# Optimization experiments

Hardware: AMD Instinct MI355X
Metric: run time of the kernel (lower is better)

Reference implementation:

```python
import jax, jax.numpy as jnp
import numpy as np

NEG_BIG = -9e15  # matches torch's -9000000000000000.0 mask value


def setup_inputs() -> dict:
    key = jax.random.key(0)
    k1, k2, k3, k4 = jax.random.split(key, 4)
    B, N, Din, Dout = 4, 4096, 256, 128
    x = jax.random.normal(k1, (B, N, Din), dtype=jnp.float32)
    adj = jax.random.randint(k2, (B, N, N), 0, 2, dtype=jnp.int32)
    weight = jax.random.normal(k3, (Din, Dout), dtype=jnp.float32) * (1.414 * (6.0 / (Din + Dout)) ** 0.5)
    a = jax.random.normal(k4, (2 * Dout, 1), dtype=jnp.float32) * 0.1
    bias = jnp.zeros((Dout,), dtype=jnp.float32)
    return {"x": x, "adj": adj, "weight": weight, "a": a, "bias": bias}


def reference(x, adj, weight, a, bias):
    Dout = weight.shape[1]
    h = jnp.matmul(x, weight)                       # [B, N, Dout]
    Wh1 = jnp.matmul(h, a[:Dout, :])                # [B, N, 1]
    Wh2 = jnp.matmul(h, a[Dout:, :])                # [B, N, 1]
    e = jax.nn.gelu(Wh1 + jnp.swapaxes(Wh2, 1, 2), approximate=False)  # [B, N, N]
    attention = jnp.where(adj > 0, e, NEG_BIG)
    attention = jax.nn.softmax(attention, axis=1)   # softmax over dim=1, as in torch code
    out = jnp.matmul(attention, h)                  # [B, N, Dout]
    out = jax.nn.gelu(out, approximate=False)
    # F.normalize(p=2, dim=1): L2-normalize over the node dimension
    norm = jnp.sqrt(jnp.sum(out * out, axis=1, keepdims=True))
    out = out / jnp.maximum(norm, 1e-12)
    return out + bias
```

## Files before the change

kernel.cpp:

```cpp
#include <hip/hip_runtime.h>
#include <hip/hip_bf16.h>
#include <stdint.h>


#define NN   4096
#define BB   4
#define DIN  256
#define DOUT 128

typedef unsigned short u16;
typedef _Float16 f16x8 __attribute__((ext_vector_type(8)));
typedef __attribute__((ext_vector_type(4))) float f32x4;

__device__ __forceinline__ u16 f2h_bits(float f) {
  _Float16 h = (_Float16)f;
  union { _Float16 h; u16 u; } v; v.h = h;
  return v.u;
}

__device__ __forceinline__ float erf_f(float x) {
  float ax = __builtin_fabsf(x);
  float t  = __builtin_amdgcn_rcpf(__builtin_fmaf(0.3275911f, ax, 1.0f));
  float p  = __builtin_fmaf(1.061405429f, t, -1.453152027f);
  p = __builtin_fmaf(p, t, 1.421413741f);
  p = __builtin_fmaf(p, t, -0.284496736f);
  p = __builtin_fmaf(p, t, 0.254829592f);
  p = p * t;
  float e  = __expf(-ax * ax);
  float er = __builtin_fmaf(-p, e, 1.0f);
  return copysignf(er, x);
}

__device__ __forceinline__ float gelu_f(float z) {
  float hz = 0.5f * z;
  return __builtin_fmaf(hz, erf_f(z * 0.70710678118654752f), hz);
}

__device__ __forceinline__ float exp_gelu(float z) { return __expf(gelu_f(z)); }

__global__ __launch_bounds__(256, 2) void k1_proj(
    const float* __restrict__ x, const float* __restrict__ weight,
    const float* __restrict__ a, u16* __restrict__ hT,
    float* __restrict__ Wh1, float* __restrict__ Wh2)
{
  __shared__ float xs[32 * 256];
  __shared__ float T[128 * 33];
  __shared__ float P2a[8 * 32], P2b[8 * 32];

  const int b = blockIdx.y, n0 = blockIdx.x * 32;
  const int tid = threadIdx.x;

  const float4* xsrc = (const float4*)(x + ((size_t)b * NN + n0) * DIN);
  float4* xd = (float4*)xs;
#pragma unroll
  for (int v = 0; v < 8; ++v) xd[tid + v * 256] = xsrc[tid + v * 256];
  __syncthreads();

  const int dg = tid & 31, rg = tid >> 5;
  float acc[4][4] = {};
  const float4* W4 = (const float4*)weight;
#pragma unroll 4
  for (int k = 0; k < 256; ++k) {
    float4 wr = W4[k * 32 + dg];
#pragma unroll
    for (int rr = 0; rr < 4; ++rr) {
      float xv = xs[(rg * 4 + rr) * 256 + k];
      acc[rr][0] = fmaf(xv, wr.x, acc[rr][0]);
      acc[rr][1] = fmaf(xv, wr.y, acc[rr][1]);
      acc[rr][2] = fmaf(xv, wr.z, acc[rr][2]);
      acc[rr][3] = fmaf(xv, wr.w, acc[rr][3]);
    }
  }
#pragma unroll
  for (int rr = 0; rr < 4; ++rr)
#pragma unroll
    for (int dd = 0; dd < 4; ++dd)
      T[(dg * 4 + dd) * 33 + rg * 4 + rr] = acc[rr][dd];
  __syncthreads();

  {
    const int d = tid & 127, half = tid >> 7;
    unsigned int uu[8];
#pragma unroll
    for (int p = 0; p < 8; ++p) {
      float f0 = T[d * 33 + half * 16 + p * 2];
      float f1 = T[d * 33 + half * 16 + p * 2 + 1];
      uu[p] = (unsigned int)f2h_bits(f0) | ((unsigned int)f2h_bits(f1) << 16);
    }
    u16* dst = hT + ((size_t)b * DOUT + d) * NN + n0 + half * 16;
    ((uint4*)dst)[0] = make_uint4(uu[0], uu[1], uu[2], uu[3]);
    ((uint4*)dst)[1] = make_uint4(uu[4], uu[5], uu[6], uu[7]);
  }
  {
    const int r = tid & 31, g8 = tid >> 5;
    float p1 = 0.f, p2 = 0.f;
#pragma unroll
    for (int q = 0; q < 16; ++q) {
      int d = g8 * 16 + q;
      float hv = T[d * 33 + r];
      p1 = fmaf(hv, a[d], p1);
      p2 = fmaf(hv, a[DOUT + d], p2);
    }
    P2a[g8 * 32 + r] = p1;
    P2b[g8 * 32 + r] = p2;
  }
  __syncthreads();
  if (tid < 32) {
    float s1 = 0.f, s2 = 0.f;
#pragma unroll
    for (int g8 = 0; g8 < 8; ++g8) { s1 += P2a[g8 * 32 + tid]; s2 += P2b[g8 * 32 + tid]; }
    Wh1[b * NN + n0 + tid] = s1;
    Wh2[b * NN + n0 + tid] = s2;
  }
}

__global__ __launch_bounds__(256) void k2a_mask(
    const int* __restrict__ adj, unsigned int* __restrict__ mask32)
{
  const int tid = threadIdx.x;
  const int row = blockIdx.x * 2 + (tid >> 7);
  const int w   = tid & 127;
  const int4* src = (const int4*)(adj + (size_t)row * NN) + w * 8;

  int4 v[8];
#pragma unroll
  for (int k = 0; k < 8; ++k) v[k] = src[k];

  unsigned int m = 0;
#pragma unroll
  for (int k = 0; k < 8; ++k) {
    m |= (v[k].x > 0 ? 1u : 0u) << (4 * k);
    m |= (v[k].y > 0 ? 1u : 0u) << (4 * k + 1);
    m |= (v[k].z > 0 ? 1u : 0u) << (4 * k + 2);
    m |= (v[k].w > 0 ? 1u : 0u) << (4 * k + 3);
  }
  mask32[(size_t)row * 128 + w] = m;
}

__global__ __launch_bounds__(256, 2) void k2b_colsum(
    const unsigned int* __restrict__ mask32, const float* __restrict__ Wh1,
    const float* __restrict__ Wh2, float* __restrict__ S)
{
  const int b = blockIdx.z, jt = blockIdx.x, ic = blockIdx.y;
  const int tid = threadIdx.x;
  const int j = jt * 256 + tid;
  const int i0 = ic * 256;
  const int jbit = tid & 31;

  const float wh2 = Wh2[b * NN + j];
  const unsigned int* mp = mask32 + ((size_t)b * NN + i0) * 128 + jt * 8 + (tid >> 5);
  const float* w1p = Wh1 + b * NN + i0;

  float s = 0.f;
  for (int g = 0; g < 32; ++g) {
    unsigned int mw[8];
    float w1v[8];
#pragma unroll
    for (int k = 0; k < 8; ++k) {
      mw[k]  = mp[(size_t)(g * 8 + k) * 128];
      w1v[k] = w1p[g * 8 + k];
    }
#pragma unroll
    for (int k = 0; k < 8; ++k) {
      float E = exp_gelu(w1v[k] + wh2);
      s += ((mw[k] >> jbit) & 1u) ? E : 0.f;
    }
  }
  atomicAdd(&S[b * NN + j], s);
}

__global__ __launch_bounds__(256) void k25_rcp(const float* __restrict__ S,
                                               float* __restrict__ Sinv)
{
  int id = blockIdx.x * 256 + threadIdx.x;
  Sinv[id] = 1.0f / S[id];
}

__global__ __launch_bounds__(256, 4) void k3_attn(
    const unsigned int* __restrict__ mask32, const float* __restrict__ Wh1,
    const float* __restrict__ Wh2, const float* __restrict__ Sinv,
    const u16* __restrict__ hT, float* __restrict__ out_pre)
{
  __shared__ __align__(16) u16 buf[4][128 * 32];

  const int b = blockIdx.y;
  const int i0 = blockIdx.x * 16;
  const int tid = threadIdx.x;
  const int w = tid >> 6, lane = tid & 63;
  const int m = lane & 15, quad = lane >> 4;
  const int i = i0 + m;

  const float w1 = Wh1[b * NN + i];
  const unsigned int* mrow = mask32 + ((size_t)b * NN + i) * 128;
  const u16* hTb = hT + (size_t)b * DOUT * NN;

  const u16* srcbase = hTb + (size_t)(lane >> 2) * NN + (lane & 3) * 8;

  f32x4 acc[8];
#pragma unroll
  for (int t = 0; t < 8; ++t) acc[t] = (f32x4){0.f, 0.f, 0.f, 0.f};

  for (int c = 0; c < 32; ++c) {
    const int j0 = w * 1024 + c * 32;

    __builtin_amdgcn_s_waitcnt(0xC07F);
#pragma unroll
    for (int inst = 0; inst < 8; ++inst) {
      const u16* g = srcbase + (size_t)inst * 16 * NN + j0;
      __builtin_amdgcn_global_load_lds(
          (const __attribute__((address_space(1))) void*)g,
          (__attribute__((address_space(3))) void*)&buf[w][inst * 512],
          16, 0, 0);
    }

    const unsigned int mb = (mrow[j0 >> 5] >> (quad * 8)) & 0xFFu;
    const int jq = j0 + quad * 8;
    const float4* wp = (const float4*)(Wh2 + b * NN + jq);
    float4 w2a = wp[0], w2b = wp[1];
    const float4* sp = (const float4*)(Sinv + b * NN + jq);
    float4 sva = sp[0], svb = sp[1];

    float q[8];
    q[0] = (mb & 1u)   ? exp_gelu(w1 + w2a.x) * sva.x : 0.f;
    q[1] = (mb & 2u)   ? exp_gelu(w1 + w2a.y) * sva.y : 0.f;
    q[2] = (mb & 4u)   ? exp_gelu(w1 + w2a.z) * sva.z : 0.f;
    q[3] = (mb & 8u)   ? exp_gelu(w1 + w2a.w) * sva.w : 0.f;
    q[4] = (mb & 16u)  ? exp_gelu(w1 + w2b.x) * svb.x : 0.f;
    q[5] = (mb & 32u)  ? exp_gelu(w1 + w2b.y) * svb.y : 0.f;
    q[6] = (mb & 64u)  ? exp_gelu(w1 + w2b.z) * svb.z : 0.f;
    q[7] = (mb & 128u) ? exp_gelu(w1 + w2b.w) * svb.w : 0.f;

    f16x8 ah, al;
#pragma unroll
    for (int e = 0; e < 8; ++e) {
      _Float16 hi = (_Float16)q[e];
      ah[e] = hi;
      al[e] = (_Float16)(q[e] - (float)hi);
    }

    __builtin_amdgcn_s_waitcnt(0x0F70);

#pragma unroll
    for (int t = 0; t < 8; ++t) {
      f16x8 bf = *(const f16x8*)&buf[w][(t * 16 + m) * 32 + quad * 8];
      acc[t] = __builtin_amdgcn_mfma_f32_16x16x32_f16(ah, bf, acc[t], 0, 0, 0);
      acc[t] = __builtin_amdgcn_mfma_f32_16x16x32_f16(al, bf, acc[t], 0, 0, 0);
    }
  }

  __syncthreads();
  float* red = (float*)&buf[0][0];
#pragma unroll
  for (int t = 0; t < 8; ++t)
#pragma unroll
    for (int r = 0; r < 4; ++r)
      red[w * 2048 + (t * 4 + r) * 64 + lane] = acc[t][r];
  __syncthreads();
#pragma unroll
  for (int tt = 0; tt < 2; ++tt) {
    const int t = w * 2 + tt;
#pragma unroll
    for (int r = 0; r < 4; ++r) {
      const int o = (t * 4 + r) * 64 + lane;
      float v = red[o] + red[2048 + o] + red[4096 + o] + red[6144 + o];
      out_pre[((size_t)b * NN + i0 + quad * 4 + r) * DOUT + t * 16 + m] = v;
    }
  }
}

__global__ __launch_bounds__(256) void k4a_gelu_norm(
    const float* __restrict__ out_pre, float* __restrict__ gout,
    float* __restrict__ norm2)
{
  __shared__ float pbuf[256];
  const int b = blockIdx.y;
  const int i0 = blockIdx.x * 64;
  const int tid = threadIdx.x;
  const int d = tid & 127, rh = tid >> 7;
  float acc = 0.f;
  for (int ii = rh; ii < 64; ii += 2) {
    size_t idx = ((size_t)b * NN + i0 + ii) * DOUT + d;
    float g = gelu_f(out_pre[idx]);
    gout[idx] = g;
    acc = fmaf(g, g, acc);
  }
  pbuf[tid] = acc;
  __syncthreads();
  if (tid < 128) atomicAdd(&norm2[b * DOUT + tid], pbuf[tid] + pbuf[tid + 128]);
}

__global__ __launch_bounds__(256) void k4b_scale(
    float* __restrict__ out, const float* __restrict__ norm2,
    const float* __restrict__ bias)
{
  int id = blockIdx.x * 256 + threadIdx.x;
  int d = id & 127;
  int b = id >> 19;
  float nrm = sqrtf(norm2[b * DOUT + d]);
  float sc = 1.0f / fmaxf(nrm, 1e-12f);
  out[id] = fmaf(out[id], sc, bias[d]);
}

extern "C" void kernel_launch(void* const* d_in, const int* in_sizes, int n_in,
                              void* d_out, int out_size, void* d_ws, size_t ws_size,
                              hipStream_t stream)
{
  const float* x      = (const float*)d_in[0];
  const int*   adj    = (const int*)d_in[1];
  const float* weight = (const float*)d_in[2];
  const float* a      = (const float*)d_in[3];
  const float* bias   = (const float*)d_in[4];
  float* out = (float*)d_out;

  char* ws = (char*)d_ws;
  u16*   hT     = (u16*)ws;
  float* Wh1    = (float*)(ws + (size_t)4 * 1024 * 1024);
  float* Wh2    = Wh1 + BB * NN;
  float* S      = Wh2 + BB * NN;
  float* Sinv   = S + BB * NN;
  unsigned int* mask32 = (unsigned int*)(Sinv + BB * NN);
  float* out_pre = (float*)((char*)mask32 + (size_t)BB * NN * 512);
  float* norm2   = out_pre + (size_t)BB * NN * DOUT;

  hipMemsetAsync(S, 0, (size_t)BB * NN * sizeof(float), stream);
  hipMemsetAsync(norm2, 0, (size_t)BB * DOUT * sizeof(float), stream);

  k1_proj<<<dim3(NN / 32, BB), 256, 0, stream>>>(x, weight, a, hT, Wh1, Wh2);
  k2a_mask<<<dim3(BB * NN / 2), 256, 0, stream>>>(adj, mask32);
  k2b_colsum<<<dim3(16, 16, BB), 256, 0, stream>>>(mask32, Wh1, Wh2, S);
  k25_rcp<<<dim3(BB * NN / 256), 256, 0, stream>>>(S, Sinv);
  k3_attn<<<dim3(NN / 16, BB), 256, 0, stream>>>(mask32, Wh1, Wh2, Sinv, hT, out_pre);
  k4a_gelu_norm<<<dim3(64, BB), 256, 0, stream>>>(out_pre, out, norm2);
  k4b_scale<<<dim3((BB * NN * DOUT) / 256), 256, 0, stream>>>(out, norm2, bias);
}
```

Measured before the change: 568.3 us.

## Fuse mask build into column-sum kernel and double row tile in attention

The separate adjacency-to-bitmask kernel is merged into the column-sum kernel. That kernel now reads adj directly, accumulates the masked softmax denominators, and builds a transposed bitmask with wave ballots. The attention kernel processes 32 rows per block instead of 16, so each staged hT tile in LDS feeds twice as many MFMAs. It reads the new column-major mask layout and lowers occupancy to 2 blocks per CU. This removes a full pass over the bitmask and halves the hT reloads, at the cost of more registers per thread and strided adj reads in the fused kernel.

```diff
diff --git a/kernel.cpp b/kernel.cpp
--- a/kernel.cpp
+++ b/kernel.cpp
@@ -114,57 +114,46 @@
   }
 }
 
-__global__ __launch_bounds__(256) void k2a_mask(
-    const int* __restrict__ adj, unsigned int* __restrict__ mask32)
-{
-  const int tid = threadIdx.x;
-  const int row = blockIdx.x * 2 + (tid >> 7);
-  const int w   = tid & 127;
-  const int4* src = (const int4*)(adj + (size_t)row * NN) + w * 8;
-
-  int4 v[8];
-#pragma unroll
-  for (int k = 0; k < 8; ++k) v[k] = src[k];
-
-  unsigned int m = 0;
-#pragma unroll
-  for (int k = 0; k < 8; ++k) {
-    m |= (v[k].x > 0 ? 1u : 0u) << (4 * k);
-    m |= (v[k].y > 0 ? 1u : 0u) << (4 * k + 1);
-    m |= (v[k].z > 0 ? 1u : 0u) << (4 * k + 2);
-    m |= (v[k].w > 0 ? 1u : 0u) << (4 * k + 3);
-  }
-  mask32[(size_t)row * 128 + w] = m;
-}
-
-__global__ __launch_bounds__(256, 2) void k2b_colsum(
-    const unsigned int* __restrict__ mask32, const float* __restrict__ Wh1,
-    const float* __restrict__ Wh2, float* __restrict__ S)
+__global__ __launch_bounds__(256, 2) void k2_fused(
+    const int* __restrict__ adj, const float* __restrict__ Wh1,
+    const float* __restrict__ Wh2, float* __restrict__ S,
+    unsigned int* __restrict__ m32)
 {
   const int b = blockIdx.z, jt = blockIdx.x, ic = blockIdx.y;
   const int tid = threadIdx.x;
   const int j = jt * 256 + tid;
-  const int i0 = ic * 256;
-  const int jbit = tid & 31;
+  const int lane = tid & 63;
+  const int jg = jt * 4 + (tid >> 6);
+  const int i0 = ic * 512;
 
   const float wh2 = Wh2[b * NN + j];
-  const unsigned int* mp = mask32 + ((size_t)b * NN + i0) * 128 + jt * 8 + (tid >> 5);
+  const int* ap = adj + ((size_t)b * NN + i0) * NN + j;
   const float* w1p = Wh1 + b * NN + i0;
+  unsigned int* mlo = m32 + ((size_t)b * 128 + jg * 2) * NN + i0;
+  unsigned int* mhi = mlo + NN;
 
   float s = 0.f;
-  for (int g = 0; g < 32; ++g) {
-    unsigned int mw[8];
-    float w1v[8];
-#pragma unroll
-    for (int k = 0; k < 8; ++k) {
-      mw[k]  = mp[(size_t)(g * 8 + k) * 128];
-      w1v[k] = w1p[g * 8 + k];
-    }
-#pragma unroll
-    for (int k = 0; k < 8; ++k) {
-      float E = exp_gelu(w1v[k] + wh2);
-      s += ((mw[k] >> jbit) & 1u) ? E : 0.f;
-    }
+  for (int g = 0; g < 8; ++g) {
+    unsigned long long acc64 = 0ull;
+#pragma unroll
+    for (int gg = 0; gg < 8; ++gg) {
+      int av[8]; float w1v[8];
+#pragma unroll
+      for (int k = 0; k < 8; ++k) {
+        const int ii = g * 64 + gg * 8 + k;
+        av[k]  = ap[(size_t)ii * NN];
+        w1v[k] = w1p[ii];
+      }
+#pragma unroll
+      for (int k = 0; k < 8; ++k) {
+        const unsigned long long bal = __ballot(av[k] > 0);
+        if (lane == gg * 8 + k) acc64 = bal;
+        const float E = exp_gelu(w1v[k] + wh2);
+        s += (av[k] > 0) ? E : 0.f;
+      }
+    }
+    mlo[g * 64 + lane] = (unsigned int)acc64;
+    mhi[g * 64 + lane] = (unsigned int)(acc64 >> 32);
   }
   atomicAdd(&S[b * NN + j], s);
 }
@@ -176,32 +165,35 @@
   Sinv[id] = 1.0f / S[id];
 }
 
-__global__ __launch_bounds__(256, 4) void k3_attn(
-    const unsigned int* __restrict__ mask32, const float* __restrict__ Wh1,
+__global__ __launch_bounds__(256, 2) void k3_attn(
+    const unsigned int* __restrict__ m32, const float* __restrict__ Wh1,
     const float* __restrict__ Wh2, const float* __restrict__ Sinv,
     const u16* __restrict__ hT, float* __restrict__ out_pre)
 {
   __shared__ __align__(16) u16 buf[4][128 * 32];
 
   const int b = blockIdx.y;
-  const int i0 = blockIdx.x * 16;
+  const int i0 = blockIdx.x * 32;
   const int tid = threadIdx.x;
   const int w = tid >> 6, lane = tid & 63;
   const int m = lane & 15, quad = lane >> 4;
-  const int i = i0 + m;
-
-  const float w1 = Wh1[b * NN + i];
-  const unsigned int* mrow = mask32 + ((size_t)b * NN + i) * 128;
+
+  const float w1a = Wh1[b * NN + i0 + m];
+  const float w1b = Wh1[b * NN + i0 + 16 + m];
+  const unsigned int* mbase = m32 + (size_t)b * 128 * NN;
   const u16* hTb = hT + (size_t)b * DOUT * NN;
-
   const u16* srcbase = hTb + (size_t)(lane >> 2) * NN + (lane & 3) * 8;
 
-  f32x4 acc[8];
-#pragma unroll
-  for (int t = 0; t < 8; ++t) acc[t] = (f32x4){0.f, 0.f, 0.f, 0.f};
+  f32x4 acc0[8], acc1[8];
+#pragma unroll
+  for (int t = 0; t < 8; ++t) {
+    acc0[t] = (f32x4){0.f, 0.f, 0.f, 0.f};
+    acc1[t] = (f32x4){0.f, 0.f, 0.f, 0.f};
+  }
 
   for (int c = 0; c < 32; ++c) {
     const int j0 = w * 1024 + c * 32;
+    const int jw = j0 >> 5;
 
     __builtin_amdgcn_s_waitcnt(0xC07F);
 #pragma unroll
@@ -213,7 +205,11 @@
           16, 0, 0);
     }
 
-    const unsigned int mb = (mrow[j0 >> 5] >> (quad * 8)) & 0xFFu;
+    const unsigned int Ma = mbase[(size_t)jw * NN + i0 + m];
+    const unsigned int Mb = mbase[(size_t)jw * NN + i0 + 16 + m];
+    const unsigned int mba = (Ma >> (quad * 8)) & 0xFFu;
+    const unsigned int mbb = (Mb >> (quad * 8)) & 0xFFu;
+
     const int jq = j0 + quad * 8;
     const float4* wp = (const float4*)(Wh2 + b * NN + jq);
     float4 w2a = wp[0], w2b = wp[1];
@@ -221,21 +217,35 @@
     float4 sva = sp[0], svb = sp[1];
 
     float q[8];
-    q[0] = (mb & 1u)   ? exp_gelu(w1 + w2a.x) * sva.x : 0.f;
-    q[1] = (mb & 2u)   ? exp_gelu(w1 + w2a.y) * sva.y : 0.f;
-    q[2] = (mb & 4u)   ? exp_gelu(w1 + w2a.z) * sva.z : 0.f;
-    q[3] = (mb & 8u)   ? exp_gelu(w1 + w2a.w) * sva.w : 0.f;
-    q[4] = (mb & 16u)  ? exp_gelu(w1 + w2b.x) * svb.x : 0.f;
-    q[5] = (mb & 32u)  ? exp_gelu(w1 + w2b.y) * svb.y : 0.f;
-    q[6] = (mb & 64u)  ? exp_gelu(w1 + w2b.z) * svb.z : 0.f;
-    q[7] = (mb & 128u) ? exp_gelu(w1 + w2b.w) * svb.w : 0.f;
-
-    f16x8 ah, al;
+    f16x8 ah_a, al_a, ah_b, al_b;
+
+    q[0] = (mba & 1u)   ? exp_gelu(w1a + w2a.x) * sva.x : 0.f;
+    q[1] = (mba & 2u)   ? exp_gelu(w1a + w2a.y) * sva.y : 0.f;
+    q[2] = (mba & 4u)   ? exp_gelu(w1a + w2a.z) * sva.z : 0.f;
+    q[3] = (mba & 8u)   ? exp_gelu(w1a + w2a.w) * sva.w : 0.f;
+    q[4] = (mba & 16u)  ? exp_gelu(w1a + w2b.x) * svb.x : 0.f;
+    q[5] = (mba & 32u)  ? exp_gelu(w1a + w2b.y) * svb.y : 0.f;
+    q[6] = (mba & 64u)  ? exp_gelu(w1a + w2b.z) * svb.z : 0.f;
+    q[7] = (mba & 128u) ? exp_gelu(w1a + w2b.w) * svb.w : 0.f;
 #pragma unroll
     for (int e = 0; e < 8; ++e) {
       _Float16 hi = (_Float16)q[e];
-      ah[e] = hi;
-      al[e] = (_Float16)(q[e] - (float)hi);
+      ah_a[e] = hi;
+      al_a[e] = (_Float16)(q[e] - (float)hi);
+    }
+    q[0] = (mbb & 1u)   ? exp_gelu(w1b + w2a.x) * sva.x : 0.f;
+    q[1] = (mbb & 2u)   ? exp_gelu(w1b + w2a.y) * sva.y : 0.f;
+    q[2] = (mbb & 4u)   ? exp_gelu(w1b + w2a.z) * sva.z : 0.f;
+    q[3] = (mbb & 8u)   ? exp_gelu(w1b + w2a.w) * sva.w : 0.f;
+    q[4] = (mbb & 16u)  ? exp_gelu(w1b + w2b.x) * svb.x : 0.f;
+    q[5] = (mbb & 32u)  ? exp_gelu(w1b + w2b.y) * svb.y : 0.f;
+    q[6] = (mbb & 64u)  ? exp_gelu(w1b + w2b.z) * svb.z : 0.f;
+    q[7] = (mbb & 128u) ? exp_gelu(w1b + w2b.w) * svb.w : 0.f;
+#pragma unroll
+    for (int e = 0; e < 8; ++e) {
+      _Float16 hi = (_Float16)q[e];
+      ah_b[e] = hi;
+      al_b[e] = (_Float16)(q[e] - (float)hi);
     }
 
     __builtin_amdgcn_s_waitcnt(0x0F70);
@@ -243,27 +253,32 @@
 #pragma unroll
     for (int t = 0; t < 8; ++t) {
       f16x8 bf = *(const f16x8*)&buf[w][(t * 16 + m) * 32 + quad * 8];
-      acc[t] = __builtin_amdgcn_mfma_f32_16x16x32_f16(ah, bf, acc[t], 0, 0, 0);
-      acc[t] = __builtin_amdgcn_mfma_f32_16x16x32_f16(al, bf, acc[t], 0, 0, 0);
-    }
-  }
-
-  __syncthreads();
+      acc0[t] = __builtin_amdgcn_mfma_f32_16x16x32_f16(ah_a, bf, acc0[t], 0, 0, 0);
+      acc0[t] = __builtin_amdgcn_mfma_f32_16x16x32_f16(al_a, bf, acc0[t], 0, 0, 0);
+      acc1[t] = __builtin_amdgcn_mfma_f32_16x16x32_f16(ah_b, bf, acc1[t], 0, 0, 0);
+      acc1[t] = __builtin_amdgcn_mfma_f32_16x16x32_f16(al_b, bf, acc1[t], 0, 0, 0);
+    }
+  }
+
   float* red = (float*)&buf[0][0];
 #pragma unroll
-  for (int t = 0; t < 8; ++t)
-#pragma unroll
-    for (int r = 0; r < 4; ++r)
-      red[w * 2048 + (t * 4 + r) * 64 + lane] = acc[t][r];
-  __syncthreads();
-#pragma unroll
-  for (int tt = 0; tt < 2; ++tt) {
-    const int t = w * 2 + tt;
-#pragma unroll
-    for (int r = 0; r < 4; ++r) {
-      const int o = (t * 4 + r) * 64 + lane;
-      float v = red[o] + red[2048 + o] + red[4096 + o] + red[6144 + o];
-      out_pre[((size_t)b * NN + i0 + quad * 4 + r) * DOUT + t * 16 + m] = v;
+  for (int rt = 0; rt < 2; ++rt) {
+    __syncthreads();
+#pragma unroll
+    for (int t = 0; t < 8; ++t)
+#pragma unroll
+      for (int r = 0; r < 4; ++r)
+        red[w * 2048 + (t * 4 + r) * 64 + lane] = rt ? acc1[t][r] : acc0[t][r];
+    __syncthreads();
+#pragma unroll
+    for (int tt = 0; tt < 2; ++tt) {
+      const int t = w * 2 + tt;
+#pragma unroll
+      for (int r = 0; r < 4; ++r) {
+        const int o = (t * 4 + r) * 64 + lane;
+        float v = red[o] + red[2048 + o] + red[4096 + o] + red[6144 + o];
+        out_pre[((size_t)b * NN + i0 + rt * 16 + quad * 4 + r) * DOUT + t * 16 + m] = v;
+      }
     }
   }
 }
@@ -318,18 +333,17 @@
   float* Wh2    = Wh1 + BB * NN;
   float* S      = Wh2 + BB * NN;
   float* Sinv   = S + BB * NN;
-  unsigned int* mask32 = (unsigned int*)(Sinv + BB * NN);
-  float* out_pre = (float*)((char*)mask32 + (size_t)BB * NN * 512);
+  unsigned int* m32 = (unsigned int*)(Sinv + BB * NN);
+  float* out_pre = (float*)((char*)m32 + (size_t)BB * 128 * NN * 4);
   float* norm2   = out_pre + (size_t)BB * NN * DOUT;
 
   hipMemsetAsync(S, 0, (size_t)BB * NN * sizeof(float), stream);
   hipMemsetAsync(norm2, 0, (size_t)BB * DOUT * sizeof(float), stream);
 
   k1_proj<<<dim3(NN / 32, BB), 256, 0, stream>>>(x, weight, a, hT, Wh1, Wh2);
-  k2a_mask<<<dim3(BB * NN / 2), 256, 0, stream>>>(adj, mask32);
-  k2b_colsum<<<dim3(16, 16, BB), 256, 0, stream>>>(mask32, Wh1, Wh2, S);
+  k2_fused<<<dim3(16, 8, BB), 256, 0, stream>>>(adj, Wh1, Wh2, S, m32);
   k25_rcp<<<dim3(BB * NN / 256), 256, 0, stream>>>(S, Sinv);
-  k3_attn<<<dim3(NN / 16, BB), 256, 0, stream>>>(mask32, Wh1, Wh2, Sinv, hT, out_pre);
+  k3_attn<<<dim3(NN / 32, BB), 256, 0, stream>>>(m32, Wh1, Wh2, Sinv, hT, out_pre);
   k4a_gelu_norm<<<dim3(64, BB), 256, 0, stream>>>(out_pre, out, norm2);
   k4b_scale<<<dim3((BB * NN * DOUT) / 256), 256, 0, stream>>>(out, norm2, bias);
 }
```

Measured after the change: 515.6 us. -9.3%, faster.
